# Performance work log

Hardware: AMD Instinct MI355X
Metric: run time of the kernel (lower is better)

## Reference

```python
import jax, jax.numpy as jnp
import numpy as np

B, L, D, T = 8, 4096, 2048, 128  # batch, seq len, hidden dim, max num targets
LN_EPS = 1e-5


def setup_inputs() -> dict:
    key = jax.random.key(0)
    ks = jax.random.split(key, 6)
    context_repr = jax.random.normal(ks[0], (B, L, D), dtype=jnp.float32)
    # varying target counts per row, max exactly T (so num_targets == T as in torch)
    counts = np.minimum((np.arange(B) * 41 + 7) % (T + 1), T)
    counts[0] = T
    counts = jnp.asarray(counts, dtype=jnp.int32)
    pos = jnp.arange(L)
    target_mask = (pos[None, :] < counts[:, None]).astype(jnp.float32)  # [B,L]
    context_mask = 1.0 - target_mask  # valid context = non-target positions
    s1 = 1.0 / np.sqrt(D)
    s2 = 1.0 / np.sqrt(2 * D)
    W1 = jax.random.uniform(ks[1], (D, 2 * D), jnp.float32, -s1, s1)
    b1 = jax.random.uniform(ks[2], (2 * D,), jnp.float32, -s1, s1)
    gamma = jnp.ones((2 * D,), jnp.float32)
    beta = jnp.zeros((2 * D,), jnp.float32)
    W2 = jax.random.uniform(ks[3], (2 * D, D), jnp.float32, -s2, s2)
    b2 = jax.random.uniform(ks[4], (D,), jnp.float32, -s2, s2)
    return {
        "context_repr": context_repr,
        "target_mask": target_mask,
        "context_mask": context_mask,
        "W1": W1, "b1": b1, "gamma": gamma, "beta": beta, "W2": W2, "b2": b2,
        "num_targets": T,
    }


def reference(context_repr, target_mask, context_mask, W1, b1, gamma, beta, W2, b2, num_targets):
    # masked mean pool: sum over ALL positions (targets assumed zeroed),
    # divide by number of valid context positions (faithful to torch code)
    ctx_count = context_mask.sum(axis=-1)                     # [B]
    ctx_sum = context_repr.sum(axis=1)                        # [B,D]
    mean = ctx_sum / jnp.maximum(ctx_count, 1.0)[:, None]
    mean = jnp.where((ctx_count > 0)[:, None], mean, 0.0)     # [B,D]
    # MLP: Linear -> GELU(exact) -> LayerNorm -> Linear
    h = jax.nn.gelu(mean @ W1 + b1, approximate=False)        # [B,2D]
    mu = h.mean(axis=-1, keepdims=True)
    var = jnp.mean((h - mu) ** 2, axis=-1, keepdims=True)
    hn = (h - mu) * jax.lax.rsqrt(var + LN_EPS) * gamma + beta
    out = hn @ W2 + b2                                        # [B,D]
    # scatter prediction into first num_tgt slots per row, rest zeros
    tgt_counts = target_mask.sum(axis=-1)                     # [B]
    valid = jnp.arange(num_targets)[None, :] < tgt_counts[:, None]  # [B,T]
    return jnp.where(valid[:, :, None], out[:, None, :], 0.0)  # [B,T,D]
```

## Files before the change

kernel.cpp:

```cpp
#include <hip/hip_runtime.h>
#include <math.h>

#define B_    8
#define L_    4096
#define D_    2048
#define D2_   4096
#define T_    128
#define LN_EPS_ 1e-5f

#define NLC    64
#define LCHUNK (L_ / NLC)
#define KC1    16
#define NK1    (D_ / KC1)
#define KC2    16
#define NK2    (D2_ / KC2)

__global__ __launch_bounds__(256)
void k_pool_masks(const float* __restrict__ x,
                  const float* __restrict__ tmask,
                  const float* __restrict__ cmask,
                  float* __restrict__ part,
                  float* __restrict__ cnt, float* __restrict__ tcnt) {
  const int lc = blockIdx.x;
  const int db = blockIdx.y;
  const int b  = blockIdx.z;
  const int tid = threadIdx.x;

  if (lc == NLC) {
    if (db != 0) return;
    float sc = 0.f, st = 0.f;
    for (int i = tid * 4; i < L_; i += 256 * 4) {
      const float4 c4 = *reinterpret_cast<const float4*>(cmask + b * L_ + i);
      const float4 t4 = *reinterpret_cast<const float4*>(tmask + b * L_ + i);
      sc += c4.x + c4.y + c4.z + c4.w;
      st += t4.x + t4.y + t4.z + t4.w;
    }
    __shared__ float sC[256], sT[256];
    sC[tid] = sc; sT[tid] = st;
    __syncthreads();
    for (int off = 128; off > 0; off >>= 1) {
      if (tid < off) { sC[tid] += sC[tid + off]; sT[tid] += sT[tid + off]; }
      __syncthreads();
    }
    if (tid == 0) { cnt[b] = sC[0]; tcnt[b] = sT[0]; }
    return;
  }

  const int d  = db * 1024 + tid * 4;
  const float* p = x + ((size_t)b * L_ + (size_t)lc * LCHUNK) * D_ + d;
  float ax = 0.f, ay = 0.f, az = 0.f, aw = 0.f;
  #pragma unroll 16
  for (int l = 0; l < LCHUNK; ++l) {
    const float4 v = *reinterpret_cast<const float4*>(p + (size_t)l * D_);
    ax += v.x; ay += v.y; az += v.z; aw += v.w;
  }
  *reinterpret_cast<float4*>(part + ((size_t)lc * B_ + b) * D_ + d) =
      make_float4(ax, ay, az, aw);
}

__global__ __launch_bounds__(256)
void k_gemv1(const float* __restrict__ part_pool,
             const float* __restrict__ W1,
             float* __restrict__ part1) {
  const int j  = blockIdx.x * 1024 + threadIdx.x * 4;
  const int ky = blockIdx.y;
  const int k0 = ky * KC1;
  __shared__ float s[B_][KC1];
  for (int i = threadIdx.x; i < B_ * KC1; i += 256) {
    const int bb = i >> 4, kk = i & (KC1 - 1);
    const float* pp = part_pool + (size_t)bb * D_ + k0 + kk;
    float v = 0.f;
    #pragma unroll 16
    for (int lc = 0; lc < NLC; ++lc) v += pp[(size_t)lc * B_ * D_];
    s[bb][kk] = v;
  }
  __syncthreads();
  float4 acc[B_];
  #pragma unroll
  for (int bb = 0; bb < B_; ++bb) acc[bb] = make_float4(0.f, 0.f, 0.f, 0.f);
  const float* w = W1 + (size_t)k0 * D2_ + j;
  #pragma unroll
  for (int k = 0; k < KC1; ++k) {
    const float4 wv = *reinterpret_cast<const float4*>(w + (size_t)k * D2_);
    #pragma unroll
    for (int bb = 0; bb < B_; ++bb) {
      const float sv = s[bb][k];
      acc[bb].x += sv * wv.x; acc[bb].y += sv * wv.y;
      acc[bb].z += sv * wv.z; acc[bb].w += sv * wv.w;
    }
  }
  #pragma unroll
  for (int bb = 0; bb < B_; ++bb)
    *reinterpret_cast<float4*>(part1 + ((size_t)ky * B_ + bb) * D2_ + j) = acc[bb];
}

__global__ __launch_bounds__(1024)
void k_gelu_ln(const float* __restrict__ part1,
               const float* __restrict__ cnt,
               const float* __restrict__ b1,
               const float* __restrict__ gamma,
               const float* __restrict__ beta,
               float* __restrict__ hn) {
  const int b = blockIdx.x;
  const int tid = threadIdx.x;
  const float c = cnt[b];
  const float scale = (c > 0.f) ? (1.f / fmaxf(c, 1.f)) : 0.f;
  const int j = tid * 4;
  float hx = 0.f, hy = 0.f, hz = 0.f, hw = 0.f;
  #pragma unroll 8
  for (int ky = 0; ky < NK1; ++ky) {
    const float4 v = *reinterpret_cast<const float4*>(
        part1 + ((size_t)ky * B_ + b) * D2_ + j);
    hx += v.x; hy += v.y; hz += v.z; hw += v.w;
  }
  const float4 bb = *reinterpret_cast<const float4*>(b1 + j);
  float g[4];
  {
    const float v0 = hx * scale + bb.x;
    const float v1 = hy * scale + bb.y;
    const float v2 = hz * scale + bb.z;
    const float v3 = hw * scale + bb.w;
    g[0] = 0.5f * v0 * (1.f + erff(v0 * 0.70710678118654752f));
    g[1] = 0.5f * v1 * (1.f + erff(v1 * 0.70710678118654752f));
    g[2] = 0.5f * v2 * (1.f + erff(v2 * 0.70710678118654752f));
    g[3] = 0.5f * v3 * (1.f + erff(v3 * 0.70710678118654752f));
  }
  float lsum = g[0] + g[1] + g[2] + g[3];
  float lsq  = g[0]*g[0] + g[1]*g[1] + g[2]*g[2] + g[3]*g[3];
  __shared__ float sS[1024], sQ[1024];
  sS[tid] = lsum; sQ[tid] = lsq;
  __syncthreads();
  for (int off = 512; off > 0; off >>= 1) {
    if (tid < off) { sS[tid] += sS[tid + off]; sQ[tid] += sQ[tid + off]; }
    __syncthreads();
  }
  const float mu  = sS[0] * (1.f / D2_);
  const float var = sQ[0] * (1.f / D2_) - mu * mu;
  const float rs  = rsqrtf(var + LN_EPS_);
  const float4 gm = *reinterpret_cast<const float4*>(gamma + j);
  const float4 bt = *reinterpret_cast<const float4*>(beta + j);
  float4 o;
  o.x = (g[0] - mu) * rs * gm.x + bt.x;
  o.y = (g[1] - mu) * rs * gm.y + bt.y;
  o.z = (g[2] - mu) * rs * gm.z + bt.z;
  o.w = (g[3] - mu) * rs * gm.w + bt.w;
  *reinterpret_cast<float4*>(hn + (size_t)b * D2_ + j) = o;
}

__global__ __launch_bounds__(256)
void k_gemv2(const float* __restrict__ HN,
             const float* __restrict__ W2,
             float* __restrict__ part2) {
  const int d  = blockIdx.x * 1024 + threadIdx.x * 4;
  const int ky = blockIdx.y;
  const int j0 = ky * KC2;
  __shared__ float s[B_][KC2];
  for (int i = threadIdx.x; i < B_ * KC2; i += 256) {
    const int bb = i >> 4, jj = i & (KC2 - 1);
    s[bb][jj] = HN[(size_t)bb * D2_ + j0 + jj];
  }
  __syncthreads();
  float4 acc[B_];
  #pragma unroll
  for (int bb = 0; bb < B_; ++bb) acc[bb] = make_float4(0.f, 0.f, 0.f, 0.f);
  const float* w = W2 + (size_t)j0 * D_ + d;
  #pragma unroll
  for (int k = 0; k < KC2; ++k) {
    const float4 wv = *reinterpret_cast<const float4*>(w + (size_t)k * D_);
    #pragma unroll
    for (int bb = 0; bb < B_; ++bb) {
      const float sv = s[bb][k];
      acc[bb].x += sv * wv.x; acc[bb].y += sv * wv.y;
      acc[bb].z += sv * wv.z; acc[bb].w += sv * wv.w;
    }
  }
  #pragma unroll
  for (int bb = 0; bb < B_; ++bb)
    *reinterpret_cast<float4*>(part2 + ((size_t)ky * B_ + bb) * D_ + d) = acc[bb];
}

__global__ __launch_bounds__(256)
void k_out(const float* __restrict__ part2,
           const float* __restrict__ b2,
           const float* __restrict__ tcnt,
           float* __restrict__ out) {
  const int b    = blockIdx.x >> 1;
  const int half = blockIdx.x & 1;
  const int d    = half * 1024 + threadIdx.x * 4;
  float ax = 0.f, ay = 0.f, az = 0.f, aw = 0.f;
  #pragma unroll 8
  for (int ky = 0; ky < NK2; ++ky) {
    const float4 v = *reinterpret_cast<const float4*>(
        part2 + ((size_t)ky * B_ + b) * D_ + d);
    ax += v.x; ay += v.y; az += v.z; aw += v.w;
  }
  const float4 bv = *reinterpret_cast<const float4*>(b2 + d);
  const float4 val = make_float4(ax + bv.x, ay + bv.y, az + bv.z, aw + bv.w);
  const float4 zero = make_float4(0.f, 0.f, 0.f, 0.f);
  const int tc = (int)(tcnt[b] + 0.5f);
  float* o = out + ((size_t)b * T_) * D_ + d;
  for (int t = 0; t < T_; ++t)
    *reinterpret_cast<float4*>(o + (size_t)t * D_) = (t < tc) ? val : zero;
}

extern "C" void kernel_launch(void* const* d_in, const int* in_sizes, int n_in,
                              void* d_out, int out_size, void* d_ws, size_t ws_size,
                              hipStream_t stream) {
  const float* context_repr = (const float*)d_in[0];
  const float* target_mask  = (const float*)d_in[1];
  const float* context_mask = (const float*)d_in[2];
  const float* W1    = (const float*)d_in[3];
  const float* b1    = (const float*)d_in[4];
  const float* gamma = (const float*)d_in[5];
  const float* beta  = (const float*)d_in[6];
  const float* W2    = (const float*)d_in[7];
  const float* b2    = (const float*)d_in[8];
  float* out = (float*)d_out;

  float* ws        = (float*)d_ws;
  float* part_pool = ws;
  float* cnt       = part_pool + (size_t)NLC * B_ * D_;
  float* tcnt      = cnt + B_;
  float* part1     = tcnt + B_;
  float* hn        = part1 + (size_t)NK1 * B_ * D2_;
  float* part2     = hn + (size_t)B_ * D2_;

  k_pool_masks<<<dim3(NLC + 1, 2, B_), dim3(256), 0, stream>>>(
      context_repr, target_mask, context_mask, part_pool, cnt, tcnt);

  k_gemv1<<<dim3(4, NK1), dim3(256), 0, stream>>>(part_pool, W1, part1);

  k_gelu_ln<<<dim3(B_), dim3(1024), 0, stream>>>(part1, cnt, b1, gamma, beta, hn);

  k_gemv2<<<dim3(2, NK2), dim3(256), 0, stream>>>(hn, W2, part2);

  k_out<<<dim3(2 * B_), dim3(256), 0, stream>>>(part2, b2, tcnt, out);
}
```

Baseline: 480.5 us.

## Add separate pool-fold kernel and double GEMV K-chunk size

A new kernel folds the 64 partial pool sums into a single context-sum buffer once. Previously every gemv1 block re-reduced its 16 columns across all 64 partials with strided, uncoalesced loads. The K-chunk size for both GEMVs doubles, which halves the number of blocks and the partial-sum traffic read by the GELU/LayerNorm and output kernels. The cost is one extra kernel launch and lower block-level parallelism in the GEMVs.

```diff
diff --git a/kernel.cpp b/kernel.cpp
--- a/kernel.cpp
+++ b/kernel.cpp
@@ -10,9 +10,9 @@
 
 #define NLC    64
 #define LCHUNK (L_ / NLC)
-#define KC1    16
+#define KC1    32
 #define NK1    (D_ / KC1)
-#define KC2    16
+#define KC2    32
 #define NK2    (D2_ / KC2)
 
 __global__ __launch_bounds__(256)
@@ -59,27 +59,37 @@
 }
 
 __global__ __launch_bounds__(256)
-void k_gemv1(const float* __restrict__ part_pool,
+void k_fold(const float* __restrict__ part,
+            float* __restrict__ ctx_sum) {
+  const int idx = (blockIdx.x * 256 + threadIdx.x) * 4;
+  float ax = 0.f, ay = 0.f, az = 0.f, aw = 0.f;
+  #pragma unroll 16
+  for (int lc = 0; lc < NLC; ++lc) {
+    const float4 v = *reinterpret_cast<const float4*>(
+        part + (size_t)lc * B_ * D_ + idx);
+    ax += v.x; ay += v.y; az += v.z; aw += v.w;
+  }
+  *reinterpret_cast<float4*>(ctx_sum + idx) = make_float4(ax, ay, az, aw);
+}
+
+__global__ __launch_bounds__(256)
+void k_gemv1(const float* __restrict__ ctx_sum,
              const float* __restrict__ W1,
              float* __restrict__ part1) {
   const int j  = blockIdx.x * 1024 + threadIdx.x * 4;
   const int ky = blockIdx.y;
   const int k0 = ky * KC1;
   __shared__ float s[B_][KC1];
-  for (int i = threadIdx.x; i < B_ * KC1; i += 256) {
-    const int bb = i >> 4, kk = i & (KC1 - 1);
-    const float* pp = part_pool + (size_t)bb * D_ + k0 + kk;
-    float v = 0.f;
-    #pragma unroll 16
-    for (int lc = 0; lc < NLC; ++lc) v += pp[(size_t)lc * B_ * D_];
-    s[bb][kk] = v;
+  if (threadIdx.x < B_ * KC1) {
+    const int bb = threadIdx.x >> 5, kk = threadIdx.x & (KC1 - 1);
+    s[bb][kk] = ctx_sum[bb * D_ + k0 + kk];
   }
   __syncthreads();
   float4 acc[B_];
   #pragma unroll
   for (int bb = 0; bb < B_; ++bb) acc[bb] = make_float4(0.f, 0.f, 0.f, 0.f);
   const float* w = W1 + (size_t)k0 * D2_ + j;
-  #pragma unroll
+  #pragma unroll 8
   for (int k = 0; k < KC1; ++k) {
     const float4 wv = *reinterpret_cast<const float4*>(w + (size_t)k * D2_);
     #pragma unroll
@@ -155,8 +165,8 @@
   const int ky = blockIdx.y;
   const int j0 = ky * KC2;
   __shared__ float s[B_][KC2];
-  for (int i = threadIdx.x; i < B_ * KC2; i += 256) {
-    const int bb = i >> 4, jj = i & (KC2 - 1);
+  if (threadIdx.x < B_ * KC2) {
+    const int bb = threadIdx.x >> 5, jj = threadIdx.x & (KC2 - 1);
     s[bb][jj] = HN[(size_t)bb * D2_ + j0 + jj];
   }
   __syncthreads();
@@ -164,7 +174,7 @@
   #pragma unroll
   for (int bb = 0; bb < B_; ++bb) acc[bb] = make_float4(0.f, 0.f, 0.f, 0.f);
   const float* w = W2 + (size_t)j0 * D_ + d;
-  #pragma unroll
+  #pragma unroll 8
   for (int k = 0; k < KC2; ++k) {
     const float4 wv = *reinterpret_cast<const float4*>(w + (size_t)k * D_);
     #pragma unroll
@@ -188,7 +198,7 @@
   const int half = blockIdx.x & 1;
   const int d    = half * 1024 + threadIdx.x * 4;
   float ax = 0.f, ay = 0.f, az = 0.f, aw = 0.f;
-  #pragma unroll 8
+  #pragma unroll 16
   for (int ky = 0; ky < NK2; ++ky) {
     const float4 v = *reinterpret_cast<const float4*>(
         part2 + ((size_t)ky * B_ + b) * D_ + d);
@@ -219,7 +229,8 @@
 
   float* ws        = (float*)d_ws;
   float* part_pool = ws;
-  float* cnt       = part_pool + (size_t)NLC * B_ * D_;
+  float* ctx_sum   = part_pool + (size_t)NLC * B_ * D_;
+  float* cnt       = ctx_sum + (size_t)B_ * D_;
   float* tcnt      = cnt + B_;
   float* part1     = tcnt + B_;
   float* hn        = part1 + (size_t)NK1 * B_ * D2_;
@@ -228,7 +239,9 @@
   k_pool_masks<<<dim3(NLC + 1, 2, B_), dim3(256), 0, stream>>>(
       context_repr, target_mask, context_mask, part_pool, cnt, tcnt);
 
-  k_gemv1<<<dim3(4, NK1), dim3(256), 0, stream>>>(part_pool, W1, part1);
+  k_fold<<<dim3((B_ * D_) / 1024), dim3(256), 0, stream>>>(part_pool, ctx_sum);
+
+  k_gemv1<<<dim3(4, NK1), dim3(256), 0, stream>>>(ctx_sum, W1, part1);
 
   k_gelu_ln<<<dim3(B_), dim3(1024), 0, stream>>>(part1, cnt, b1, gamma, beta, hn);
 
```

Result: faster. 469.1 us (-2.4%).
